# Kernel optimization log

Measured on AMD Instinct MI355X. Metric: run time of the kernel, lower is better.

## Reference

```python
import jax, jax.numpy as jnp
import numpy as np
import math

D_MODEL = 1024
N_HEADS = 16
D_K = D_MODEL // N_HEADS
LN_EPS = 1e-5


def _linear_params(key, d_in, d_out):
    # torch Linear stores weight as [out, in]; xavier_uniform init
    bound = math.sqrt(6.0 / (d_in + d_out))
    kw, kb = jax.random.split(key)
    W = jax.random.uniform(kw, (d_out, d_in), jnp.float32, -bound, bound)
    b = jnp.zeros((d_out,), jnp.float32)
    return W, b


def setup_inputs() -> dict:
    key = jax.random.key(0)
    ks = jax.random.split(key, 8)
    x = jax.random.normal(ks[0], (2, 2048, D_MODEL), jnp.float32)
    reasoning_state = jax.random.normal(ks[1], (2, D_MODEL), jnp.float32)
    Wq, bq = _linear_params(ks[2], D_MODEL, D_MODEL)
    Wk, bk = _linear_params(ks[3], D_MODEL, D_MODEL)
    Wv, bv = _linear_params(ks[4], D_MODEL, D_MODEL)
    Wr, br = _linear_params(ks[5], D_MODEL, D_MODEL)
    Wo, bo = _linear_params(ks[6], D_MODEL, D_MODEL)
    ln_g = jnp.ones((D_MODEL,), jnp.float32)
    ln_b = jnp.zeros((D_MODEL,), jnp.float32)
    return {"x": x, "reasoning_state": reasoning_state,
            "Wq": Wq, "bq": bq, "Wk": Wk, "bk": bk, "Wv": Wv, "bv": bv,
            "Wr": Wr, "br": br, "Wo": Wo, "bo": bo, "ln_g": ln_g, "ln_b": ln_b}


def reference(x, reasoning_state, Wq, bq, Wk, bk, Wv, bv, Wr, br, Wo, bo, ln_g, ln_b):
    B, S, D = x.shape
    H, dk = N_HEADS, D_K

    def proj(z, W, b):  # torch Linear: z @ W.T + b
        return z @ W.T + b

    # [B, H, S, dk]
    Q = proj(x, Wq, bq).reshape(B, S, H, dk).transpose(0, 2, 1, 3)
    K = proj(x, Wk, bk).reshape(B, S, H, dk).transpose(0, 2, 1, 3)
    V = proj(x, Wv, bv).reshape(B, S, H, dk).transpose(0, 2, 1, 3)

    scores = jnp.einsum('bhsd,bhtd->bhst', Q, K) / math.sqrt(dk)

    # reasoning bias: R is [B, H, 1, dk]; Q @ R^T -> [B, H, S, 1], broadcast over keys
    R = proj(reasoning_state, Wr, br).reshape(B, 1, H, dk).transpose(0, 2, 1, 3)
    scores = scores + jnp.einsum('bhsd,bhud->bhsu', Q, R)  # u == 1, broadcasts

    attn = jax.nn.softmax(scores, axis=-1)
    context = jnp.einsum('bhst,bhtd->bshd', attn, V).reshape(B, S, D)
    out = proj(context, Wo, bo)

    # residual + LayerNorm
    y = out + x
    mu = jnp.mean(y, axis=-1, keepdims=True)
    var = jnp.var(y, axis=-1, keepdims=True)
    y = (y - mu) * jax.lax.rsqrt(var + LN_EPS) * ln_g + ln_b
    return (y, attn)
```

## Files before the change

### kernel.cpp

```cpp
#include <hip/hip_runtime.h>
#include <hip/hip_bf16.h>

#define DM 1024
#define NH 16
#define DKK 64
#define SL 2048
#define NBATCH 2
#define NR (NBATCH*SL)

typedef __attribute__((ext_vector_type(8))) __bf16 bf16x8;
typedef __attribute__((ext_vector_type(4))) float f32x4;
using bf16 = __hip_bfloat16;

#define QSCALE 0.18033688011112042f

__global__ __launch_bounds__(256) void cvt_kernel(const float* __restrict__ src,
                                                  bf16* __restrict__ dst, int n4) {
  int stride = gridDim.x * blockDim.x;
  for (int i = blockIdx.x * blockDim.x + threadIdx.x; i < n4; i += stride) {
    float4 v = ((const float4*)src)[i];
    union { bf16 h[4]; ushort4 u; } un;
    un.h[0] = __float2bfloat16(v.x);
    un.h[1] = __float2bfloat16(v.y);
    un.h[2] = __float2bfloat16(v.z);
    un.h[3] = __float2bfloat16(v.w);
    ((ushort4*)dst)[i] = un.u;
  }
}

__global__ __launch_bounds__(256) void cvt4_kernel(
    const float* __restrict__ s0, const float* __restrict__ s1,
    const float* __restrict__ s2, const float* __restrict__ s3,
    bf16* __restrict__ d0, bf16* __restrict__ d1,
    bf16* __restrict__ d2, bf16* __restrict__ d3) {
  const int z = blockIdx.y;
  const float* src = (z == 0) ? s0 : (z == 1) ? s1 : (z == 2) ? s2 : s3;
  bf16* dst = (z == 0) ? d0 : (z == 1) ? d1 : (z == 2) ? d2 : d3;
  const int n4 = DM * DM / 4;
  int stride = gridDim.x * blockDim.x;
  for (int i = blockIdx.x * blockDim.x + threadIdx.x; i < n4; i += stride) {
    float4 v = ((const float4*)src)[i];
    union { bf16 h[4]; ushort4 u; } un;
    un.h[0] = __float2bfloat16(v.x);
    un.h[1] = __float2bfloat16(v.y);
    un.h[2] = __float2bfloat16(v.z);
    un.h[3] = __float2bfloat16(v.w);
    ((ushort4*)dst)[i] = un.u;
  }
}

__device__ __forceinline__ void gemm_core(const bf16* __restrict__ A, const bf16* __restrict__ W,
                                          int rowStart, int colStart,
                                          bf16* As, bf16* Bs, f32x4 acc[4][4]) {
  const int t = threadIdx.x;
  const int lane = t & 63, w = t >> 6;
  const int lg = lane & 15, lh = lane >> 4;
  const int wm = (w >> 1) * 64, wn = (w & 1) * 64;
#pragma unroll
  for (int i = 0; i < 4; ++i)
#pragma unroll
    for (int j = 0; j < 4; ++j) acc[i][j] = (f32x4){0.f, 0.f, 0.f, 0.f};

  for (int kt = 0; kt < DM / 32; ++kt) {
    int kb = kt * 32;
#pragma unroll
    for (int q = 0; q < 2; ++q) {
      int idx = q * 256 + t;
      int row = idx >> 2;
      int ce = (idx & 3) * 8;
      const bf16* ga = A + (size_t)(rowStart + row) * DM + kb + ce;
      const bf16* gb = W + (size_t)(colStart + row) * DM + kb + ce;
      int ldsbase = (q * 256 + w * 64) * 8;
      __builtin_amdgcn_global_load_lds((const __attribute__((address_space(1))) void*)ga,
                                       (__attribute__((address_space(3))) void*)(As + ldsbase),
                                       16, 0, 0);
      __builtin_amdgcn_global_load_lds((const __attribute__((address_space(1))) void*)gb,
                                       (__attribute__((address_space(3))) void*)(Bs + ldsbase),
                                       16, 0, 0);
    }
    __syncthreads();
    bf16x8 af[4], bfr[4];
#pragma unroll
    for (int i = 0; i < 4; ++i)
      af[i] = *(const bf16x8*)(As + (wm + i * 16 + lg) * 32 + 8 * lh);
#pragma unroll
    for (int j = 0; j < 4; ++j)
      bfr[j] = *(const bf16x8*)(Bs + (wn + j * 16 + lg) * 32 + 8 * lh);
#pragma unroll
    for (int i = 0; i < 4; ++i)
#pragma unroll
      for (int j = 0; j < 4; ++j)
        acc[i][j] = __builtin_amdgcn_mfma_f32_16x16x32_bf16(af[i], bfr[j], acc[i][j], 0, 0, 0);
    __syncthreads();
  }
}

__global__ __launch_bounds__(256) void gemm_qkv_kernel(
    const bf16* __restrict__ xb,
    const bf16* __restrict__ Wqb, const bf16* __restrict__ Wkb, const bf16* __restrict__ Wvb,
    const float* __restrict__ bq, const float* __restrict__ bk, const float* __restrict__ bv,
    bf16* __restrict__ Qb, bf16* __restrict__ Kb, bf16* __restrict__ Vt) {
  __shared__ bf16 smem[128 * 128];
  bf16* As = smem;
  bf16* Bs = smem + 4096;
  const int z = blockIdx.z;
  const bf16* W = (z == 0) ? Wqb : (z == 1) ? Wkb : Wvb;
  const float* bias = (z == 0) ? bq : (z == 1) ? bk : bv;
  int rowStart = blockIdx.y * 128, colStart = blockIdx.x * 128;
  f32x4 acc[4][4];
  gemm_core(xb, W, rowStart, colStart, As, Bs, acc);

  const int t = threadIdx.x, lane = t & 63, w = t >> 6;
  const int lg = lane & 15, lh = lane >> 4;
  const int wm = (w >> 1) * 64, wn = (w & 1) * 64;
  if (z < 2) {
    bf16* out = (z == 0) ? Qb : Kb;
    const float sc = (z == 0) ? QSCALE : 1.0f;
#pragma unroll
    for (int i = 0; i < 4; ++i)
#pragma unroll
      for (int j = 0; j < 4; ++j) {
        int col = colStart + wn + j * 16 + lg;
        float bb = bias[col];
#pragma unroll
        for (int r = 0; r < 4; ++r) {
          int row = rowStart + wm + i * 16 + 4 * lh + r;
          out[(size_t)row * DM + col] = __float2bfloat16((acc[i][j][r] + bb) * sc);
        }
      }
  } else {
    char* T = (char*)smem;
#pragma unroll
    for (int i = 0; i < 4; ++i)
#pragma unroll
      for (int j = 0; j < 4; ++j) {
        int col = wn + j * 16 + lg;
        float bb = bias[colStart + col];
        const int swz = (col & 7) << 4;
#pragma unroll
        for (int r2 = 0; r2 < 4; r2 += 2) {
          int row = wm + i * 16 + 4 * lh + r2;
          union { bf16 hh[2]; unsigned u; } un;
          un.hh[0] = __float2bfloat16(acc[i][j][r2] + bb);
          un.hh[1] = __float2bfloat16(acc[i][j][r2 + 1] + bb);
          *(unsigned*)(T + ((col * 256 + row * 2) ^ swz)) = un.u;
        }
      }
    __syncthreads();
    const int b_i = rowStart >> 11;
    const int sbase = rowStart & 2047;
#pragma unroll
    for (int rd = 0; rd < 8; ++rd) {
      int d_loc = rd * 16 + (t >> 4);
      int s8 = (t & 15) * 8;
      bf16x8 v = *(const bf16x8*)(T + ((d_loc * 256 + s8 * 2) ^ ((d_loc & 7) << 4)));
      int col = colStart + d_loc;
      int h2 = col >> 6, d = col & 63;
      *(bf16x8*)(Vt + ((size_t)(b_i * NH + h2) * DKK + d) * SL + sbase + s8) = v;
    }
  }
}

__global__ __launch_bounds__(512, 2) void attn2_kernel(
    const bf16* __restrict__ Qb, const bf16* __restrict__ Kb, const bf16* __restrict__ Vt,
    float* __restrict__ attn_out, bf16* __restrict__ ctxb) {
  __shared__ bf16 Ps[32 * 2048];
  __shared__ float sl_s[8 * 32];
  __shared__ float linv_s[32];
  const int t = threadIdx.x, lane = t & 63, w = t >> 6;
  const int lg = lane & 15, lh = lane >> 4;

  const int L = blockIdx.x;
  const int xcd = L & 7, idx = L >> 3;
  const int bh = xcd * 4 + (idx >> 6);
  const int qt = idx & 63;
  const int b = bh >> 4, h = bh & 15;
  const int qbase = qt * 32;

  const bf16* Kbase = Kb + (size_t)b * SL * DM + h * DKK;
  const bf16* Vtb = Vt + (size_t)bh * DKK * SL;
  char* Pb = (char*)Ps;
  const int kw = w * 256;

  bf16x8 qf[2][2];
#pragma unroll
  for (int i = 0; i < 2; ++i)
#pragma unroll
    for (int ks = 0; ks < 2; ++ks)
      qf[i][ks] = *(const bf16x8*)(Qb +
          (size_t)(b * SL + qbase + i * 16 + lg) * DM + h * DKK + ks * 32 + 8 * lh);

  float lsum[2] = {0.f, 0.f};
  for (int kt = 0; kt < 8; ++kt) {
    const int kb = kw + kt * 32;
    bf16x8 kf[2][2];
#pragma unroll
    for (int jj = 0; jj < 2; ++jj)
#pragma unroll
      for (int ks = 0; ks < 2; ++ks)
        kf[jj][ks] = *(const bf16x8*)(Kbase +
            (size_t)(kb + jj * 16 + lg) * DM + ks * 32 + 8 * lh);
    f32x4 s[2][2];
    __builtin_amdgcn_s_setprio(1);
#pragma unroll
    for (int i = 0; i < 2; ++i)
#pragma unroll
      for (int jj = 0; jj < 2; ++jj) {
        f32x4 z = (f32x4){0.f, 0.f, 0.f, 0.f};
        z = __builtin_amdgcn_mfma_f32_16x16x32_bf16(kf[jj][0], qf[i][0], z, 0, 0, 0);
        s[i][jj] = __builtin_amdgcn_mfma_f32_16x16x32_bf16(kf[jj][1], qf[i][1], z, 0, 0, 0);
      }
    __builtin_amdgcn_s_setprio(0);
#pragma unroll
    for (int i = 0; i < 2; ++i) {
      const int q = i * 16 + lg;
      const int swz = (q & 7) << 4;
#pragma unroll
      for (int jj = 0; jj < 2; ++jj) {
        const int key0 = kb + jj * 16 + 4 * lh;
        float p0 = exp2f(s[i][jj][0]);
        float p1 = exp2f(s[i][jj][1]);
        float p2 = exp2f(s[i][jj][2]);
        float p3 = exp2f(s[i][jj][3]);
        lsum[i] += (p0 + p1) + (p2 + p3);
        union { bf16 hh[4]; ushort4 u4; } un;
        un.hh[0] = __float2bfloat16(p0);
        un.hh[1] = __float2bfloat16(p1);
        un.hh[2] = __float2bfloat16(p2);
        un.hh[3] = __float2bfloat16(p3);
        *(ushort4*)(Pb + ((q * 4096 + key0 * 2) ^ swz)) = un.u4;
      }
    }
  }
#pragma unroll
  for (int i = 0; i < 2; ++i) {
    lsum[i] += __shfl_xor(lsum[i], 16);
    lsum[i] += __shfl_xor(lsum[i], 32);
  }
  if (lh == 0) {
    sl_s[w * 32 + lg] = lsum[0];
    sl_s[w * 32 + 16 + lg] = lsum[1];
  }
  __syncthreads();
  if (t < 32) {
    float tot = 0.f;
#pragma unroll
    for (int w8 = 0; w8 < 8; ++w8) tot += sl_s[w8 * 32 + t];
    linv_s[t] = 1.f / tot;
  }
  __syncthreads();

  float* attn_base = attn_out + (size_t)bh * SL * SL + (size_t)qbase * SL;
#pragma unroll
  for (int rd = 0; rd < 16; ++rd) {
    int id2 = rd * 512 + t;
    int q = id2 >> 8;
    int kcol = (id2 & 255) * 8;
    union { bf16x8 v; ushort us[8]; } pu;
    pu.v = *(const bf16x8*)(Pb + ((q * 4096 + kcol * 2) ^ ((q & 7) << 4)));
    float li = linv_s[q];
    f32x4 lo, hi;
#pragma unroll
    for (int e = 0; e < 4; ++e) {
      lo[e] = __uint_as_float((unsigned)pu.us[e] << 16) * li;
      hi[e] = __uint_as_float((unsigned)pu.us[e + 4] << 16) * li;
    }
    f32x4* dst = (f32x4*)(attn_base + (size_t)q * SL + kcol);
    __builtin_nontemporal_store(lo, dst);
    __builtin_nontemporal_store(hi, dst + 1);
  }

  f32x4 acc[2][4];
#pragma unroll
  for (int i = 0; i < 2; ++i)
#pragma unroll
    for (int jd = 0; jd < 4; ++jd) acc[i][jd] = (f32x4){0.f, 0.f, 0.f, 0.f};
  for (int ks8 = 0; ks8 < 8; ++ks8) {
    const int kb = kw + ks8 * 32;
    bf16x8 pf[2];
#pragma unroll
    for (int i = 0; i < 2; ++i) {
      const int q = i * 16 + lg;
      pf[i] = *(const bf16x8*)(Pb + ((q * 4096 + (kb + 8 * lh) * 2) ^ ((q & 7) << 4)));
    }
    bf16x8 vf[4];
#pragma unroll
    for (int jd = 0; jd < 4; ++jd)
      vf[jd] = *(const bf16x8*)(Vtb + (size_t)(jd * 16 + lg) * SL + kb + 8 * lh);
    __builtin_amdgcn_s_setprio(1);
#pragma unroll
    for (int i = 0; i < 2; ++i)
#pragma unroll
      for (int jd = 0; jd < 4; ++jd)
        acc[i][jd] = __builtin_amdgcn_mfma_f32_16x16x32_bf16(pf[i], vf[jd], acc[i][jd], 0, 0, 0);
    __builtin_amdgcn_s_setprio(0);
  }
  __syncthreads();

  float* part = (float*)Ps;
#pragma unroll
  for (int i = 0; i < 2; ++i)
#pragma unroll
    for (int jd = 0; jd < 4; ++jd)
#pragma unroll
      for (int r = 0; r < 4; ++r)
        part[w * 2048 + (i * 16 + 4 * lh + r) * 64 + jd * 16 + lg] = acc[i][jd][r];
  __syncthreads();

  {
    int e = t * 4;
    int q = e >> 6, d0 = e & 63;
    f32x4 sum = (f32x4){0.f, 0.f, 0.f, 0.f};
#pragma unroll
    for (int w8 = 0; w8 < 8; ++w8) sum += *(const f32x4*)(part + w8 * 2048 + e);
    float li = linv_s[q];
    union { bf16 hh[4]; ushort4 u4; } un;
#pragma unroll
    for (int r = 0; r < 4; ++r) un.hh[r] = __float2bfloat16(sum[r] * li);
    *(ushort4*)(ctxb + (size_t)(b * SL + qbase + q) * DM + h * DKK + d0) = un.u4;
  }
}

__global__ __launch_bounds__(256) void gemm_o_kernel(
    const bf16* __restrict__ ctxb, const bf16* __restrict__ Wob, const float* __restrict__ bo,
    const float* __restrict__ xf, float* __restrict__ ypre) {
  __shared__ bf16 As[128 * 32], Bs[64 * 32];
  const int t = threadIdx.x, lane = t & 63, w = t >> 6;
  const int lg = lane & 15, lh = lane >> 4;
  const int wm = (w >> 1) * 64, wn = (w & 1) * 32;
  int rowStart = blockIdx.y * 128, colStart = blockIdx.x * 64;
  f32x4 acc[4][2];
#pragma unroll
  for (int i = 0; i < 4; ++i)
#pragma unroll
    for (int j = 0; j < 2; ++j) acc[i][j] = (f32x4){0.f, 0.f, 0.f, 0.f};

  for (int kt = 0; kt < DM / 32; ++kt) {
    int kb = kt * 32;
#pragma unroll
    for (int q = 0; q < 2; ++q) {
      int idx = q * 256 + t;
      int row = idx >> 2;
      int ce = (idx & 3) * 8;
      const bf16* ga = ctxb + (size_t)(rowStart + row) * DM + kb + ce;
      int ldsbase = (q * 256 + w * 64) * 8;
      __builtin_amdgcn_global_load_lds((const __attribute__((address_space(1))) void*)ga,
                                       (__attribute__((address_space(3))) void*)(As + ldsbase),
                                       16, 0, 0);
    }
    {
      int row = t >> 2, ce = (t & 3) * 8;
      const bf16* gb = Wob + (size_t)(colStart + row) * DM + kb + ce;
      int ldsbase = (w * 64) * 8;
      __builtin_amdgcn_global_load_lds((const __attribute__((address_space(1))) void*)gb,
                                       (__attribute__((address_space(3))) void*)(Bs + ldsbase),
                                       16, 0, 0);
    }
    __syncthreads();
    bf16x8 af[4], bfr[2];
#pragma unroll
    for (int i = 0; i < 4; ++i)
      af[i] = *(const bf16x8*)(As + (wm + i * 16 + lg) * 32 + 8 * lh);
#pragma unroll
    for (int j = 0; j < 2; ++j)
      bfr[j] = *(const bf16x8*)(Bs + (wn + j * 16 + lg) * 32 + 8 * lh);
#pragma unroll
    for (int i = 0; i < 4; ++i)
#pragma unroll
      for (int j = 0; j < 2; ++j)
        acc[i][j] = __builtin_amdgcn_mfma_f32_16x16x32_bf16(af[i], bfr[j], acc[i][j], 0, 0, 0);
    __syncthreads();
  }
#pragma unroll
  for (int i = 0; i < 4; ++i)
#pragma unroll
    for (int j = 0; j < 2; ++j) {
      int col = colStart + wn + j * 16 + lg;
      float bb = bo[col];
#pragma unroll
      for (int r = 0; r < 4; ++r) {
        int row = rowStart + wm + i * 16 + 4 * lh + r;
        ypre[(size_t)row * DM + col] = acc[i][j][r] + bb + xf[(size_t)row * DM + col];
      }
    }
}

__global__ __launch_bounds__(256) void ln_kernel(const float* __restrict__ ypre,
                                                 const float* __restrict__ g,
                                                 const float* __restrict__ bta,
                                                 float* __restrict__ out) {
  int row = blockIdx.x;
  const float* yr = ypre + (size_t)row * DM;
  int t = threadIdx.x;
  float4 v = *(const float4*)(yr + t * 4);
  float s = v.x + v.y + v.z + v.w;
  float ss = v.x * v.x + v.y * v.y + v.z * v.z + v.w * v.w;
#pragma unroll
  for (int off = 1; off < 64; off <<= 1) {
    s += __shfl_xor(s, off);
    ss += __shfl_xor(ss, off);
  }
  __shared__ float red[8];
  int w = t >> 6, lane = t & 63;
  if (lane == 0) { red[w] = s; red[4 + w] = ss; }
  __syncthreads();
  s = red[0] + red[1] + red[2] + red[3];
  ss = red[4] + red[5] + red[6] + red[7];
  float mu = s * (1.f / (float)DM);
  float var = ss * (1.f / (float)DM) - mu * mu;
  float rstd = rsqrtf(var + 1e-5f);
  float4 gv = *(const float4*)(g + t * 4);
  float4 bv = *(const float4*)(bta + t * 4);
  float4 o;
  o.x = (v.x - mu) * rstd * gv.x + bv.x;
  o.y = (v.y - mu) * rstd * gv.y + bv.y;
  o.z = (v.z - mu) * rstd * gv.z + bv.z;
  o.w = (v.w - mu) * rstd * gv.w + bv.w;
  *(float4*)(out + (size_t)row * DM + t * 4) = o;
}

extern "C" void kernel_launch(void* const* d_in, const int* in_sizes, int n_in,
                              void* d_out, int out_size, void* d_ws, size_t ws_size,
                              hipStream_t stream) {
  (void)in_sizes; (void)n_in; (void)out_size; (void)ws_size;
  const float* x = (const float*)d_in[0];
  const float* Wq = (const float*)d_in[2];
  const float* bq = (const float*)d_in[3];
  const float* Wk = (const float*)d_in[4];
  const float* bk = (const float*)d_in[5];
  const float* Wv = (const float*)d_in[6];
  const float* bv = (const float*)d_in[7];
  const float* Wo = (const float*)d_in[10];
  const float* bo = (const float*)d_in[11];
  const float* ln_g = (const float*)d_in[12];
  const float* ln_b = (const float*)d_in[13];
  float* out = (float*)d_out;

  char* ws = (char*)d_ws;
  const size_t MB = 1ull << 20;
  bf16* xb   = (bf16*)(ws + 0 * MB);
  bf16* Wqb  = (bf16*)(ws + 8 * MB);
  bf16* Wkb  = (bf16*)(ws + 10 * MB);
  bf16* Wvb  = (bf16*)(ws + 12 * MB);
  bf16* Wob  = (bf16*)(ws + 14 * MB);
  bf16* Qb   = (bf16*)(ws + 16 * MB);
  bf16* Kb   = (bf16*)(ws + 24 * MB);
  bf16* Vt   = (bf16*)(ws + 32 * MB);
  bf16* ctxb = (bf16*)(ws + 40 * MB);
  float* ypre = (float*)(ws + 48 * MB);

  float* y_out = out;
  float* attn_out = out + (size_t)NR * DM;

  cvt_kernel<<<2048, 256, 0, stream>>>(x, xb, NR * DM / 4);
  cvt4_kernel<<<dim3(256, 4), 256, 0, stream>>>(Wq, Wk, Wv, Wo, Wqb, Wkb, Wvb, Wob);

  gemm_qkv_kernel<<<dim3(8, 32, 3), 256, 0, stream>>>(xb, Wqb, Wkb, Wvb, bq, bk, bv, Qb, Kb, Vt);
  attn2_kernel<<<2048, 512, 0, stream>>>(Qb, Kb, Vt, attn_out, ctxb);
  gemm_o_kernel<<<dim3(16, 32), 256, 0, stream>>>(ctxb, Wob, bo, x, ypre);
  ln_kernel<<<4096, 256, 0, stream>>>(ypre, ln_g, ln_b, y_out);
}
```

Baseline: 316.7 us.

## Halve attention query tile to raise occupancy and compute row sums from LDS

Each attention block now handles 16 query rows instead of 32, with half the LDS probability buffer, launch bounds raised to 4 blocks per CU and twice as many blocks. Row sums are computed per wave from the stored bf16 probabilities with a wave shuffle reduction, replacing the per-lane partial sums and the cross-wave reduction pass. Barriers become explicit lgkmcnt waits plus s_barrier. The aim is more latency hiding through occupancy, at the cost of loading K and V twice as often per query and normalising with rounded bf16 sums.

```diff
diff --git a/kernel.cpp b/kernel.cpp
--- a/kernel.cpp
+++ b/kernel.cpp
@@ -13,6 +13,12 @@
 using bf16 = __hip_bfloat16;
 
 #define QSCALE 0.18033688011112042f
+
+#define LGKM_BARRIER() do { \
+  asm volatile("s_waitcnt lgkmcnt(0)" ::: "memory"); \
+  __builtin_amdgcn_s_barrier(); \
+  __builtin_amdgcn_sched_barrier(0); \
+} while (0)
 
 __global__ __launch_bounds__(256) void cvt_kernel(const float* __restrict__ src,
                                                   bf16* __restrict__ dst, int n4) {
@@ -130,6 +136,7 @@
       }
   } else {
     char* T = (char*)smem;
+    __syncthreads();
 #pragma unroll
     for (int i = 0; i < 4; ++i)
 #pragma unroll
@@ -161,163 +168,125 @@
   }
 }
 
-__global__ __launch_bounds__(512, 2) void attn2_kernel(
+__global__ __launch_bounds__(512, 4) void attn_fused_kernel(
     const bf16* __restrict__ Qb, const bf16* __restrict__ Kb, const bf16* __restrict__ Vt,
     float* __restrict__ attn_out, bf16* __restrict__ ctxb) {
-  __shared__ bf16 Ps[32 * 2048];
-  __shared__ float sl_s[8 * 32];
-  __shared__ float linv_s[32];
+  __shared__ bf16 Ps[16 * 2048];
+  __shared__ float linv_s[16];
   const int t = threadIdx.x, lane = t & 63, w = t >> 6;
   const int lg = lane & 15, lh = lane >> 4;
-
   const int L = blockIdx.x;
-  const int xcd = L & 7, idx = L >> 3;
-  const int bh = xcd * 4 + (idx >> 6);
-  const int qt = idx & 63;
+  const int xcd = L & 7, r_ = L >> 3;
+  const int bh = xcd * 4 + (r_ >> 7);
+  const int tile = r_ & 127;
   const int b = bh >> 4, h = bh & 15;
-  const int qbase = qt * 32;
+  const int qbase = tile * 16;
+  const int kw = w * 256;
+  char* Pb = (char*)Ps;
+
+  bf16x8 qf[2];
+#pragma unroll
+  for (int ks = 0; ks < 2; ++ks)
+    qf[ks] = *(const bf16x8*)(Qb +
+        (size_t)(b * SL + qbase + lg) * DM + h * DKK + ks * 32 + 8 * lh);
 
   const bf16* Kbase = Kb + (size_t)b * SL * DM + h * DKK;
   const bf16* Vtb = Vt + (size_t)bh * DKK * SL;
-  char* Pb = (char*)Ps;
-  const int kw = w * 256;
-
-  bf16x8 qf[2][2];
-#pragma unroll
-  for (int i = 0; i < 2; ++i)
-#pragma unroll
-    for (int ks = 0; ks < 2; ++ks)
-      qf[i][ks] = *(const bf16x8*)(Qb +
-          (size_t)(b * SL + qbase + i * 16 + lg) * DM + h * DKK + ks * 32 + 8 * lh);
-
-  float lsum[2] = {0.f, 0.f};
-  for (int kt = 0; kt < 8; ++kt) {
-    const int kb = kw + kt * 32;
-    bf16x8 kf[2][2];
-#pragma unroll
-    for (int jj = 0; jj < 2; ++jj)
-#pragma unroll
-      for (int ks = 0; ks < 2; ++ks)
-        kf[jj][ks] = *(const bf16x8*)(Kbase +
-            (size_t)(kb + jj * 16 + lg) * DM + ks * 32 + 8 * lh);
-    f32x4 s[2][2];
+  float* attn_base = attn_out + (size_t)bh * SL * SL + (size_t)qbase * SL;
+
+  for (int j = 0; j < 16; ++j) {
+    const int key = kw + j * 16;
+    bf16x8 kf0 = *(const bf16x8*)(Kbase + (size_t)(key + lg) * DM + 8 * lh);
+    bf16x8 kf1 = *(const bf16x8*)(Kbase + (size_t)(key + lg) * DM + 32 + 8 * lh);
+    f32x4 z = (f32x4){0.f, 0.f, 0.f, 0.f};
+    z = __builtin_amdgcn_mfma_f32_16x16x32_bf16(kf0, qf[0], z, 0, 0, 0);
+    f32x4 s = __builtin_amdgcn_mfma_f32_16x16x32_bf16(kf1, qf[1], z, 0, 0, 0);
+    union { bf16 hh[4]; ushort4 u4; } un;
+    un.hh[0] = __float2bfloat16(exp2f(s[0]));
+    un.hh[1] = __float2bfloat16(exp2f(s[1]));
+    un.hh[2] = __float2bfloat16(exp2f(s[2]));
+    un.hh[3] = __float2bfloat16(exp2f(s[3]));
+    *(ushort4*)(Pb + ((lg * 4096 + (key + 4 * lh) * 2) ^ ((lg & 7) << 4))) = un.u4;
+  }
+  LGKM_BARRIER();
+
+#pragma unroll
+  for (int rr = 0; rr < 2; ++rr) {
+    const int row = w * 2 + rr;
+    const int swz = (row & 7) << 4;
+    bf16x8 prow[4];
+    float ssum = 0.f;
+#pragma unroll
+    for (int cc = 0; cc < 4; ++cc) {
+      prow[cc] = *(const bf16x8*)(Pb + (row * 4096 + (((cc * 64 + lane) * 16) ^ swz)));
+      union { bf16x8 v; ushort us[8]; } pu;
+      pu.v = prow[cc];
+#pragma unroll
+      for (int e = 0; e < 8; ++e)
+        ssum += __uint_as_float((unsigned)pu.us[e] << 16);
+    }
+#pragma unroll
+    for (int off = 1; off < 64; off <<= 1) ssum += __shfl_xor(ssum, off);
+    const float li = 1.f / ssum;
+    if (lane == 0) linv_s[row] = li;
+    float* rowbase = attn_base + (size_t)row * SL;
+#pragma unroll
+    for (int cc = 0; cc < 4; ++cc) {
+      union { bf16x8 v; ushort us[8]; } pu;
+      pu.v = prow[cc];
+      f32x4 lo, hi;
+#pragma unroll
+      for (int e = 0; e < 4; ++e) {
+        lo[e] = __uint_as_float((unsigned)pu.us[e] << 16) * li;
+        hi[e] = __uint_as_float((unsigned)pu.us[e + 4] << 16) * li;
+      }
+      f32x4* dst = (f32x4*)(rowbase + (cc * 64 + lane) * 8);
+      __builtin_nontemporal_store(lo, dst);
+      __builtin_nontemporal_store(hi, dst + 1);
+    }
+  }
+
+  f32x4 cacc[4];
+#pragma unroll
+  for (int jd = 0; jd < 4; ++jd) cacc[jd] = (f32x4){0.f, 0.f, 0.f, 0.f};
+#pragma unroll
+  for (int ks = 0; ks < 8; ++ks) {
+    const int kcol = kw + ks * 32 + 8 * lh;
+    bf16x8 pf = *(const bf16x8*)(Pb + ((lg * 4096 + kcol * 2) ^ ((lg & 7) << 4)));
+    bf16x8 vf[4];
+#pragma unroll
+    for (int jd = 0; jd < 4; ++jd)
+      vf[jd] = *(const bf16x8*)(Vtb + (size_t)(jd * 16 + lg) * SL + kcol);
     __builtin_amdgcn_s_setprio(1);
 #pragma unroll
-    for (int i = 0; i < 2; ++i)
-#pragma unroll
-      for (int jj = 0; jj < 2; ++jj) {
-        f32x4 z = (f32x4){0.f, 0.f, 0.f, 0.f};
-        z = __builtin_amdgcn_mfma_f32_16x16x32_bf16(kf[jj][0], qf[i][0], z, 0, 0, 0);
-        s[i][jj] = __builtin_amdgcn_mfma_f32_16x16x32_bf16(kf[jj][1], qf[i][1], z, 0, 0, 0);
-      }
+    for (int jd = 0; jd < 4; ++jd)
+      cacc[jd] = __builtin_amdgcn_mfma_f32_16x16x32_bf16(pf, vf[jd], cacc[jd], 0, 0, 0);
     __builtin_amdgcn_s_setprio(0);
-#pragma unroll
-    for (int i = 0; i < 2; ++i) {
-      const int q = i * 16 + lg;
-      const int swz = (q & 7) << 4;
-#pragma unroll
-      for (int jj = 0; jj < 2; ++jj) {
-        const int key0 = kb + jj * 16 + 4 * lh;
-        float p0 = exp2f(s[i][jj][0]);
-        float p1 = exp2f(s[i][jj][1]);
-        float p2 = exp2f(s[i][jj][2]);
-        float p3 = exp2f(s[i][jj][3]);
-        lsum[i] += (p0 + p1) + (p2 + p3);
-        union { bf16 hh[4]; ushort4 u4; } un;
-        un.hh[0] = __float2bfloat16(p0);
-        un.hh[1] = __float2bfloat16(p1);
-        un.hh[2] = __float2bfloat16(p2);
-        un.hh[3] = __float2bfloat16(p3);
-        *(ushort4*)(Pb + ((q * 4096 + key0 * 2) ^ swz)) = un.u4;
-      }
-    }
-  }
-#pragma unroll
-  for (int i = 0; i < 2; ++i) {
-    lsum[i] += __shfl_xor(lsum[i], 16);
-    lsum[i] += __shfl_xor(lsum[i], 32);
-  }
-  if (lh == 0) {
-    sl_s[w * 32 + lg] = lsum[0];
-    sl_s[w * 32 + 16 + lg] = lsum[1];
-  }
-  __syncthreads();
-  if (t < 32) {
-    float tot = 0.f;
-#pragma unroll
-    for (int w8 = 0; w8 < 8; ++w8) tot += sl_s[w8 * 32 + t];
-    linv_s[t] = 1.f / tot;
-  }
-  __syncthreads();
-
-  float* attn_base = attn_out + (size_t)bh * SL * SL + (size_t)qbase * SL;
-#pragma unroll
-  for (int rd = 0; rd < 16; ++rd) {
-    int id2 = rd * 512 + t;
-    int q = id2 >> 8;
-    int kcol = (id2 & 255) * 8;
-    union { bf16x8 v; ushort us[8]; } pu;
-    pu.v = *(const bf16x8*)(Pb + ((q * 4096 + kcol * 2) ^ ((q & 7) << 4)));
-    float li = linv_s[q];
-    f32x4 lo, hi;
-#pragma unroll
-    for (int e = 0; e < 4; ++e) {
-      lo[e] = __uint_as_float((unsigned)pu.us[e] << 16) * li;
-      hi[e] = __uint_as_float((unsigned)pu.us[e + 4] << 16) * li;
-    }
-    f32x4* dst = (f32x4*)(attn_base + (size_t)q * SL + kcol);
-    __builtin_nontemporal_store(lo, dst);
-    __builtin_nontemporal_store(hi, dst + 1);
-  }
-
-  f32x4 acc[2][4];
-#pragma unroll
-  for (int i = 0; i < 2; ++i)
-#pragma unroll
-    for (int jd = 0; jd < 4; ++jd) acc[i][jd] = (f32x4){0.f, 0.f, 0.f, 0.f};
-  for (int ks8 = 0; ks8 < 8; ++ks8) {
-    const int kb = kw + ks8 * 32;
-    bf16x8 pf[2];
-#pragma unroll
-    for (int i = 0; i < 2; ++i) {
-      const int q = i * 16 + lg;
-      pf[i] = *(const bf16x8*)(Pb + ((q * 4096 + (kb + 8 * lh) * 2) ^ ((q & 7) << 4)));
-    }
-    bf16x8 vf[4];
-#pragma unroll
-    for (int jd = 0; jd < 4; ++jd)
-      vf[jd] = *(const bf16x8*)(Vtb + (size_t)(jd * 16 + lg) * SL + kb + 8 * lh);
-    __builtin_amdgcn_s_setprio(1);
-#pragma unroll
-    for (int i = 0; i < 2; ++i)
-#pragma unroll
-      for (int jd = 0; jd < 4; ++jd)
-        acc[i][jd] = __builtin_amdgcn_mfma_f32_16x16x32_bf16(pf[i], vf[jd], acc[i][jd], 0, 0, 0);
-    __builtin_amdgcn_s_setprio(0);
-  }
-  __syncthreads();
+  }
+  LGKM_BARRIER();
 
   float* part = (float*)Ps;
 #pragma unroll
-  for (int i = 0; i < 2; ++i)
-#pragma unroll
-    for (int jd = 0; jd < 4; ++jd)
-#pragma unroll
-      for (int r = 0; r < 4; ++r)
-        part[w * 2048 + (i * 16 + 4 * lh + r) * 64 + jd * 16 + lg] = acc[i][jd][r];
-  __syncthreads();
+  for (int jd = 0; jd < 4; ++jd)
+#pragma unroll
+    for (int r = 0; r < 4; ++r)
+      part[w * 1024 + (4 * lh + r) * 64 + jd * 16 + lg] = cacc[jd][r];
+  LGKM_BARRIER();
 
   {
-    int e = t * 4;
-    int q = e >> 6, d0 = e & 63;
-    f32x4 sum = (f32x4){0.f, 0.f, 0.f, 0.f};
-#pragma unroll
-    for (int w8 = 0; w8 < 8; ++w8) sum += *(const f32x4*)(part + w8 * 2048 + e);
-    float li = linv_s[q];
-    union { bf16 hh[4]; ushort4 u4; } un;
-#pragma unroll
-    for (int r = 0; r < 4; ++r) un.hh[r] = __float2bfloat16(sum[r] * li);
-    *(ushort4*)(ctxb + (size_t)(b * SL + qbase + q) * DM + h * DKK + d0) = un.u4;
+    const int e = t * 2;
+    const int row = e >> 6, col = e & 63;
+    float s0 = 0.f, s1 = 0.f;
+#pragma unroll
+    for (int w8 = 0; w8 < 8; ++w8) {
+      s0 += part[w8 * 1024 + e];
+      s1 += part[w8 * 1024 + e + 1];
+    }
+    const float li = linv_s[row];
+    union { bf16 hh[2]; unsigned u; } un;
+    un.hh[0] = __float2bfloat16(s0 * li);
+    un.hh[1] = __float2bfloat16(s1 * li);
+    *(unsigned*)(ctxb + (size_t)(b * SL + qbase + row) * DM + h * DKK + col) = un.u;
   }
 }
 
@@ -456,7 +425,7 @@
   cvt4_kernel<<<dim3(256, 4), 256, 0, stream>>>(Wq, Wk, Wv, Wo, Wqb, Wkb, Wvb, Wob);
 
   gemm_qkv_kernel<<<dim3(8, 32, 3), 256, 0, stream>>>(xb, Wqb, Wkb, Wvb, bq, bk, bv, Qb, Kb, Vt);
-  attn2_kernel<<<2048, 512, 0, stream>>>(Qb, Kb, Vt, attn_out, ctxb);
+  attn_fused_kernel<<<4096, 512, 0, stream>>>(Qb, Kb, Vt, attn_out, ctxb);
   gemm_o_kernel<<<dim3(16, 32), 256, 0, stream>>>(ctxb, Wob, bo, x, ypre);
   ln_kernel<<<4096, 256, 0, stream>>>(ypre, ln_g, ln_b, y_out);
 }
```

Measured after the change: 374.4 us. 1.18x slower.
